# Kernel tuning notes

Measured on AMD Instinct MI355X. Metric: run time of the kernel, lower is better.

## Reference

```python
import jax, jax.numpy as jnp
import numpy as np

HEADS = 8
DIM = 512
DIM_HEAD = DIM // 8        # 64
M = DIM // 2               # 256 landmarks
PINV_ITERS = 6
KERNEL = 33                # residual depthwise conv kernel (33,1)


def moore_penrose_pinv(x, iters):
    # x: [b, h, m, m]; Newton-Schulz style iterative pseudoinverse (lucidrains impl)
    abs_x = jnp.abs(x)
    col = abs_x.sum(axis=-1)
    row = abs_x.sum(axis=-2)
    z = jnp.swapaxes(x, -1, -2) / (jnp.max(col) * jnp.max(row))
    I = jnp.eye(x.shape[-1], dtype=x.dtype)
    for _ in range(iters):
        xz = x @ z
        z = 0.25 * z @ (13.0 * I - xz @ (15.0 * I - xz @ (7.0 * I - xz)))
    return z


def setup_inputs() -> dict:
    key = jax.random.key(0)
    ks = jax.random.split(key, 5)
    b, n, dim = 4, 8192, DIM
    x = jax.random.normal(ks[0], (b, n, dim), dtype=jnp.float32)
    # to_qkv: Linear(dim, 3*inner_dim, bias=False); inner_dim = heads*dim_head = dim
    w_qkv = jax.random.normal(ks[1], (dim, 3 * dim), dtype=jnp.float32) / np.sqrt(dim)
    # to_out: Linear(inner_dim, dim) with bias (dropout = identity in eval)
    w_out = jax.random.normal(ks[2], (dim, dim), dtype=jnp.float32) / np.sqrt(dim)
    b_out = jax.random.normal(ks[3], (dim,), dtype=jnp.float32) * 0.01
    # res_conv: Conv2d(heads, heads, (33,1), padding=(16,0), groups=heads, bias=False)
    conv_w = jax.random.normal(ks[4], (HEADS, 1, KERNEL, 1), dtype=jnp.float32) / np.sqrt(KERNEL)
    return {"x": x, "w_qkv": w_qkv, "w_out": w_out, "b_out": b_out, "conv_w": conv_w}


def nystrom_attention(x, w_qkv, w_out, b_out, conv_w):
    b, n, dim = x.shape
    h, d, m = HEADS, DIM_HEAD, M
    # pad front so seq len divisible by num_landmarks (no-op for n=8192, m=256)
    pad = (m - n % m) % m
    xp = jnp.pad(x, ((0, 0), (pad, 0), (0, 0)))
    np_ = n + pad

    qkv = xp @ w_qkv                                   # [b, np, 3*dim]
    q, k, v = jnp.split(qkv, 3, axis=-1)
    to_heads = lambda t: t.reshape(b, np_, h, d).transpose(0, 2, 1, 3)  # [b,h,np,d]
    q, k, v = to_heads(q), to_heads(k), to_heads(v)
    q = q * (d ** -0.5)

    l = np_ // m                                       # tokens per landmark
    pool = lambda t: t.reshape(b, h, m, l, d).mean(axis=3)  # [b,h,m,d]
    q_l, k_l = pool(q), pool(k)

    attn1 = jax.nn.softmax(jnp.einsum('bhnd,bhmd->bhnm', q, k_l), axis=-1)    # [b,h,np,m]
    attn2 = jax.nn.softmax(jnp.einsum('bhid,bhjd->bhij', q_l, k_l), axis=-1)  # [b,h,m,m]
    attn3 = jax.nn.softmax(jnp.einsum('bhmd,bhnd->bhmn', q_l, k), axis=-1)    # [b,h,m,np]

    attn2_inv = moore_penrose_pinv(attn2, PINV_ITERS)
    out = (attn1 @ attn2_inv) @ (attn3 @ v)            # [b,h,np,d]

    # depthwise conv residual over the sequence axis, per head
    res = jax.lax.conv_general_dilated(
        v, conv_w, window_strides=(1, 1),
        padding=((KERNEL // 2, KERNEL // 2), (0, 0)),
        dimension_numbers=('NCHW', 'OIHW', 'NCHW'),
        feature_group_count=h)
    out = out + res

    out = out.transpose(0, 2, 1, 3).reshape(b, np_, dim)
    out = out @ w_out + b_out
    return out[:, -n:]


def reference(x, w_qkv, w_out, b_out, conv_w):
    return x + nystrom_attention(x, w_qkv, w_out, b_out, conv_w)
```

## Files before the change

### kernel.cpp

```cpp
#include <hip/hip_runtime.h>


#define N_SEQ 8192
#define DMODEL 512
#define NHEAD 8
#define DHEAD 64
#define NLAND 256
#define BH 32

typedef unsigned short u16;
typedef __attribute__((ext_vector_type(8))) short bh8;
typedef __attribute__((ext_vector_type(4))) float fx4;

__device__ __forceinline__ float bf2f(u16 u) { return __uint_as_float(((unsigned)u) << 16); }
__device__ __forceinline__ u16 f2bf(float f) {
    unsigned x = __float_as_uint(f);
    return (u16)((x + 0x7fffu + ((x >> 16) & 1u)) >> 16);
}
__device__ __forceinline__ fx4 mfma16(bh8 a, bh8 b, fx4 c) {
    return __builtin_amdgcn_mfma_f32_16x16x32_bf16(a, b, c, 0, 0, 0);
}
__device__ __forceinline__ void gload16(u16* lds, const u16* g) {
    __builtin_amdgcn_global_load_lds(
        (const __attribute__((address_space(1))) unsigned int*)g,
        (__attribute__((address_space(3))) unsigned int*)lds, 16, 0, 0);
}

__global__ void detect_kernel(const u16* __restrict__ X, unsigned* scal)
{
    __shared__ int cnt;
    if (threadIdx.x == 0) cnt = 0;
    if (threadIdx.x == 0) scal[0] = 0x3f800000u;
    if (threadIdx.x == 1) scal[1] = 0u;
    __syncthreads();
    u16 u = X[threadIdx.x * 2];
    int e = (u >> 7) & 0xFF;
    int insane = (u != 0) && (e < 90 || e > 140);
    atomicAdd(&cnt, insane);
    __syncthreads();
    if (threadIdx.x == 0) scal[2] = (cnt > 64) ? 1u : 0u;
}

__global__ __launch_bounds__(256) void convert4_kernel(
    const void* __restrict__ in, u16* __restrict__ out, int n4, const unsigned* __restrict__ flag)
{
    int i = blockIdx.x * 256 + threadIdx.x;
    if (i >= n4) return;
    if (flag[0]) {
        float4 v = ((const float4*)in)[i];
        ushort4 o;
        o.x = f2bf(v.x); o.y = f2bf(v.y); o.z = f2bf(v.z); o.w = f2bf(v.w);
        ((ushort4*)out)[i] = o;
    } else {
        ((ushort4*)out)[i] = ((const ushort4*)in)[i];
    }
}

__global__ void small_convert_kernel(
    const void* __restrict__ b_in, u16* __restrict__ b_out,
    const void* __restrict__ c_in, u16* __restrict__ c_out,
    const unsigned* __restrict__ flag)
{
    int t = threadIdx.x;
    unsigned f = flag[0];
    const void* in; u16* out; int i;
    if (t < 128)       { in = b_in; out = b_out; i = t; }
    else if (t < 194)  { in = c_in; out = c_out; i = t - 128; }
    else return;
    if (f) {
        float4 v = ((const float4*)in)[i];
        ushort4 o;
        o.x = f2bf(v.x); o.y = f2bf(v.y); o.z = f2bf(v.z); o.w = f2bf(v.w);
        ((ushort4*)out)[i] = o;
    } else {
        ((ushort4*)out)[i] = ((const ushort4*)in)[i];
    }
}

__global__ __launch_bounds__(256) void wtrans2_kernel(
    const void* __restrict__ in1, u16* __restrict__ out1,
    const void* __restrict__ in2, u16* __restrict__ out2,
    const unsigned* __restrict__ flag)
{
    int idx = blockIdx.x * 256 + threadIdx.x;
    unsigned f = flag[0];
    if (idx < 786432) {
        int r = idx / 1536, c = idx % 1536;
        float v = f ? ((const float*)in1)[idx] : bf2f(((const u16*)in1)[idx]);
        out1[(size_t)c * 512 + r] = f2bf(v);
    } else {
        int k = idx - 786432;
        int r = k >> 9, c = k & 511;
        float v = f ? ((const float*)in2)[k] : bf2f(((const u16*)in2)[k]);
        out2[(size_t)c * 512 + r] = f2bf(v);
    }
}

__global__ __launch_bounds__(256) void qkv_mfma_kernel(
    const u16* __restrict__ X, const u16* __restrict__ WT,
    u16* __restrict__ Q, u16* __restrict__ K, u16* __restrict__ VT)
{
    __shared__ __align__(16) u16 SH[128 * 136 + 64];
    u16* Xs = SH;
    u16* Ws = SH + 8192;
    const int tid = threadIdx.x;
    const int wave = tid >> 6, lane = tid & 63;
    const int wrow = (wave >> 1) * 64, wcol = (wave & 1) * 64;
    const int i0 = blockIdx.x * 128;
    const int j0 = blockIdx.y * 128;
    const int la = lane >> 3, lb = lane & 7;
    const int lm = lane & 15, lq = lane >> 4;
    const int sw = lm & 7;
    const int sc = (lb ^ la) * 8;
    fx4 acc[4][4];
#pragma unroll
    for (int a = 0; a < 4; ++a)
#pragma unroll
        for (int b = 0; b < 4; ++b) acc[a][b] = (fx4){0.f, 0.f, 0.f, 0.f};

    for (int k0 = 0; k0 < DMODEL; k0 += 64) {
        __syncthreads();
#pragma unroll
        for (int jj = 0; jj < 4; ++jj) {
            int rb = wave * 32 + jj * 8;
            gload16(Xs + rb * 64, X + (size_t)(i0 + rb + la) * DMODEL + k0 + sc);
            gload16(Ws + rb * 64, WT + (size_t)(j0 + rb + la) * DMODEL + k0 + sc);
        }
        __syncthreads();
#pragma unroll
        for (int ks = 0; ks < 2; ++ks) {
            const int po = ((ks * 4 + lq) ^ sw) * 8;
            bh8 xf[4], wf[4];
#pragma unroll
            for (int im = 0; im < 4; ++im)
                xf[im] = *(const bh8*)(Xs + (wrow + im * 16 + lm) * 64 + po);
#pragma unroll
            for (int in = 0; in < 4; ++in)
                wf[in] = *(const bh8*)(Ws + (wcol + in * 16 + lm) * 64 + po);
#pragma unroll
            for (int im = 0; im < 4; ++im)
#pragma unroll
                for (int in = 0; in < 4; ++in)
                    acc[im][in] = mfma16(wf[in], xf[im], acc[im][in]);
        }
    }

    const int j0V = j0 - 1024;
    if (j0V >= 0) {
        __syncthreads();
#pragma unroll
        for (int im = 0; im < 4; ++im) {
            int nl = wrow + im * 16 + lm;
#pragma unroll
            for (int in = 0; in < 4; ++in) {
                int cl = wcol + in * 16 + (lq << 2);
#pragma unroll
                for (int r = 0; r < 4; ++r)
                    SH[(cl + r) * 136 + nl] = f2bf(acc[im][in][r]);
            }
        }
        __syncthreads();
        const int bb = i0 >> 13, ns0 = i0 & (N_SEQ - 1);
        const size_t rowg0 = (size_t)bb * 512 + j0V;
        const int nof = (tid & 15) * 8;
        const int c0 = tid >> 4;
#pragma unroll
        for (int j = 0; j < 8; ++j) {
            int c = c0 + j * 16;
            uint4 v = *(const uint4*)(SH + c * 136 + nof);
            *(uint4*)(VT + (rowg0 + c) * N_SEQ + ns0 + nof) = v;
        }
    } else {
#pragma unroll
        for (int im = 0; im < 4; ++im) {
            int m = i0 + wrow + im * 16 + lm;
            int bb = m >> 13, ns = m & (N_SEQ - 1);
#pragma unroll
            for (int in = 0; in < 4; ++in) {
                int nn = j0 + wcol + in * 16 + (lq << 2);
                int which = nn >> 9;
                int h = (nn >> 6) & 7;
                int d = nn & 63;
                u16* dst = (which == 0) ? Q : K;
                float s = (which == 0) ? 0.125f : 1.f;
                ushort4 o;
                o.x = f2bf(acc[im][in][0] * s); o.y = f2bf(acc[im][in][1] * s);
                o.z = f2bf(acc[im][in][2] * s); o.w = f2bf(acc[im][in][3] * s);
                *(ushort4*)(dst + ((size_t)(bb * NHEAD + h) * N_SEQ + ns) * DHEAD + d) = o;
            }
        }
    }
}

__global__ __launch_bounds__(64) void pool_kernel(
    const u16* __restrict__ Q, const u16* __restrict__ K,
    float* __restrict__ QL, float* __restrict__ KL,
    u16* __restrict__ QLb, u16* __restrict__ KLb)
{
    int m = blockIdx.x, bh = blockIdx.y, d = threadIdx.x;
    size_t base = ((size_t)bh * N_SEQ + m * 32) * DHEAD + d;
    float sq = 0.f, sk = 0.f;
#pragma unroll
    for (int i = 0; i < 32; ++i) {
        sq += bf2f(Q[base + i * DHEAD]);
        sk += bf2f(K[base + i * DHEAD]);
    }
    size_t ob = ((size_t)bh * NLAND + m) * DHEAD + d;
    sq *= (1.f / 32.f); sk *= (1.f / 32.f);
    QL[ob] = sq; KL[ob] = sk;
    QLb[ob] = f2bf(sq); KLb[ob] = f2bf(sk);
}

__global__ __launch_bounds__(256) void attn2_kernel(
    const float* __restrict__ QL, const float* __restrict__ KL, float* __restrict__ A2)
{
    __shared__ float qrow[64];
    __shared__ float red[256];
    int i = blockIdx.x, bh = blockIdx.y, j = threadIdx.x;
    if (j < 64) qrow[j] = QL[((size_t)bh * NLAND + i) * DHEAD + j];
    __syncthreads();
    const float* kr = KL + ((size_t)bh * NLAND + j) * DHEAD;
    float lg = 0.f;
#pragma unroll
    for (int d = 0; d < 64; ++d) lg += qrow[d] * kr[d];
    red[j] = lg; __syncthreads();
    for (int s = 128; s > 0; s >>= 1) { if (j < s) red[j] = fmaxf(red[j], red[j + s]); __syncthreads(); }
    float mx = red[0]; __syncthreads();
    float p = __expf(lg - mx);
    red[j] = p; __syncthreads();
    for (int s = 128; s > 0; s >>= 1) { if (j < s) red[j] += red[j + s]; __syncthreads(); }
    float sum = red[0];
    A2[((size_t)bh * NLAND + i) * NLAND + j] = p / sum;
}

__global__ __launch_bounds__(256) void absmax_kernel(const float* __restrict__ A2, unsigned* scal)
{
    __shared__ float red[256];
    int bh = blockIdx.x, t = threadIdx.x;
    const float* Ab = A2 + (size_t)bh * 65536;
    float rs = 0.f;
    for (int i = 0; i < 256; ++i) rs += fabsf(Ab[i * 256 + t]);
    red[t] = rs; __syncthreads();
    for (int s = 128; s > 0; s >>= 1) { if (t < s) red[t] = fmaxf(red[t], red[t + s]); __syncthreads(); }
    if (t == 0) atomicMax(scal + 1, __float_as_uint(red[0]));
}

__global__ __launch_bounds__(256) void z0_kernel(
    const float* __restrict__ A2, const unsigned* __restrict__ scal,
    u16* __restrict__ zb, u16* __restrict__ zbT, u16* __restrict__ A2b)
{
    float inv = 1.f / (__uint_as_float(scal[0]) * __uint_as_float(scal[1]));
    size_t idx = (size_t)blockIdx.x * 256 + threadIdx.x;
    size_t bh = idx >> 16;
    int r = (int)(idx & 65535);
    int i = r >> 8, j = r & 255;
    float a = A2[idx];
    zb[idx]  = f2bf(A2[(bh << 16) + (size_t)j * 256 + i] * inv);
    zbT[idx] = f2bf(a * inv);
    A2b[idx] = f2bf(a);
}

__global__ __launch_bounds__(256) void bgemm_mfma_kernel(
    const u16* __restrict__ A, const u16* __restrict__ BT,
    u16* __restrict__ Cn, u16* __restrict__ Ct, const u16* __restrict__ E,
    int N, long sB, long sCn, long sCt, float sc, float alpha, float beta, int wn, int wt)
{
    __shared__ u16 As[64 * 72];
    __shared__ u16 Bs[64 * 72];
    const int tid = threadIdx.x;
    const int wave = tid >> 6, lane = tid & 63;
    const int wm = (wave >> 1) * 32, wnn = (wave & 1) * 32;
    const int i0 = blockIdx.x * 64, j0 = blockIdx.y * 64, bh = blockIdx.z;
    const u16* Ab = A + (size_t)bh * 65536;
    const u16* Bb = BT + (size_t)bh * sB;
    const int srow = tid >> 2, scol = (tid & 3) * 16;
    const int lm = lane & 15, lq = lane >> 4;
    fx4 acc[2][2];
#pragma unroll
    for (int a = 0; a < 2; ++a)
#pragma unroll
        for (int b = 0; b < 2; ++b) acc[a][b] = (fx4){0.f, 0.f, 0.f, 0.f};

    for (int k0 = 0; k0 < 256; k0 += 64) {
        uint4 a0 = *(const uint4*)(Ab + (size_t)(i0 + srow) * 256 + k0 + scol);
        uint4 a1 = *(const uint4*)(Ab + (size_t)(i0 + srow) * 256 + k0 + scol + 8);
        uint4 b0 = *(const uint4*)(Bb + (size_t)(j0 + srow) * 256 + k0 + scol);
        uint4 b1 = *(const uint4*)(Bb + (size_t)(j0 + srow) * 256 + k0 + scol + 8);
        __syncthreads();
        *(uint4*)(As + srow * 72 + scol) = a0;
        *(uint4*)(As + srow * 72 + scol + 8) = a1;
        *(uint4*)(Bs + srow * 72 + scol) = b0;
        *(uint4*)(Bs + srow * 72 + scol + 8) = b1;
        __syncthreads();
#pragma unroll
        for (int ks = 0; ks < 2; ++ks) {
            bh8 lf[2], rf[2];
#pragma unroll
            for (int im = 0; im < 2; ++im)
                lf[im] = *(const bh8*)(As + (wm + im * 16 + lm) * 72 + ks * 32 + lq * 8);
#pragma unroll
            for (int in = 0; in < 2; ++in)
                rf[in] = *(const bh8*)(Bs + (wnn + in * 16 + lm) * 72 + ks * 32 + lq * 8);
#pragma unroll
            for (int im = 0; im < 2; ++im)
#pragma unroll
                for (int in = 0; in < 2; ++in)
                    acc[im][in] = mfma16(lf[im], rf[in], acc[im][in]);
        }
    }
#pragma unroll
    for (int im = 0; im < 2; ++im) {
#pragma unroll
        for (int in = 0; in < 2; ++in) {
            int n = j0 + wnn + in * 16 + lm;
            int m0 = i0 + wm + im * 16 + (lq << 2);
            float c[4];
#pragma unroll
            for (int r = 0; r < 4; ++r) {
                int m = m0 + r;
                float x = beta * acc[im][in][r];
                if (alpha != 0.f)
                    x += alpha * bf2f(E[(size_t)bh * 65536 + (size_t)m * 256 + n]);
                if (m == n) x += sc;
                c[r] = x;
            }
            if (wn) {
#pragma unroll
                for (int r = 0; r < 4; ++r)
                    Cn[(size_t)bh * sCn + (size_t)(m0 + r) * N + n] = f2bf(c[r]);
            }
            if (wt) {
                ushort4 o;
                o.x = f2bf(c[0]); o.y = f2bf(c[1]); o.z = f2bf(c[2]); o.w = f2bf(c[3]);
                *(ushort4*)(Ct + (size_t)bh * sCt + (size_t)n * 256 + m0) = o;
            }
        }
    }
}

__global__ __launch_bounds__(256) void bgemm_pair_kernel(
    const u16* __restrict__ Az, const u16* __restrict__ Au, const u16* __restrict__ BT,
    u16* __restrict__ Czn, u16* __restrict__ Cun, u16* __restrict__ CunT)
{
    __shared__ u16 As[64 * 72];
    __shared__ u16 Bs[64 * 72];
    const int tid = threadIdx.x;
    const int wave = tid >> 6, lane = tid & 63;
    const int wm = (wave >> 1) * 32, wnn = (wave & 1) * 32;
    const int i0 = blockIdx.x * 64, j0 = blockIdx.y * 64;
    const int bz = blockIdx.z;
    const int bh = bz & 31;
    const int isU = bz >> 5;
    const u16* Ab = (isU ? Au : Az) + (size_t)bh * 65536;
    const u16* Bb = BT + (size_t)bh * 65536;
    const int srow = tid >> 2, scol = (tid & 3) * 16;
    const int lm = lane & 15, lq = lane >> 4;
    fx4 acc[2][2];
#pragma unroll
    for (int a = 0; a < 2; ++a)
#pragma unroll
        for (int b = 0; b < 2; ++b) acc[a][b] = (fx4){0.f, 0.f, 0.f, 0.f};

    for (int k0 = 0; k0 < 256; k0 += 64) {
        uint4 a0 = *(const uint4*)(Ab + (size_t)(i0 + srow) * 256 + k0 + scol);
        uint4 a1 = *(const uint4*)(Ab + (size_t)(i0 + srow) * 256 + k0 + scol + 8);
        uint4 b0 = *(const uint4*)(Bb + (size_t)(j0 + srow) * 256 + k0 + scol);
        uint4 b1 = *(const uint4*)(Bb + (size_t)(j0 + srow) * 256 + k0 + scol + 8);
        __syncthreads();
        *(uint4*)(As + srow * 72 + scol) = a0;
        *(uint4*)(As + srow * 72 + scol + 8) = a1;
        *(uint4*)(Bs + srow * 72 + scol) = b0;
        *(uint4*)(Bs + srow * 72 + scol + 8) = b1;
        __syncthreads();
#pragma unroll
        for (int ks = 0; ks < 2; ++ks) {
            bh8 lf[2], rf[2];
#pragma unroll
            for (int im = 0; im < 2; ++im)
                lf[im] = *(const bh8*)(As + (wm + im * 16 + lm) * 72 + ks * 32 + lq * 8);
#pragma unroll
            for (int in = 0; in < 2; ++in)
                rf[in] = *(const bh8*)(Bs + (wnn + in * 16 + lm) * 72 + ks * 32 + lq * 8);
#pragma unroll
            for (int im = 0; im < 2; ++im)
#pragma unroll
                for (int in = 0; in < 2; ++in)
                    acc[im][in] = mfma16(lf[im], rf[in], acc[im][in]);
        }
    }
#pragma unroll
    for (int im = 0; im < 2; ++im) {
#pragma unroll
        for (int in = 0; in < 2; ++in) {
            int n = j0 + wnn + in * 16 + lm;
            int m0 = i0 + wm + im * 16 + (lq << 2);
            float c[4];
#pragma unroll
            for (int r = 0; r < 4; ++r) c[r] = 0.25f * acc[im][in][r];
            u16* rows = isU ? Cun : Czn;
#pragma unroll
            for (int r = 0; r < 4; ++r)
                rows[(size_t)bh * 65536 + (size_t)(m0 + r) * 256 + n] = f2bf(c[r]);
            if (isU) {
                ushort4 o;
                o.x = f2bf(c[0]); o.y = f2bf(c[1]); o.z = f2bf(c[2]); o.w = f2bf(c[3]);
                *(ushort4*)(CunT + (size_t)bh * 65536 + (size_t)n * 256 + m0) = o;
            }
        }
    }
}

__global__ __launch_bounds__(256, 2) void attn3v_mfma_kernel(
    const u16* __restrict__ QLb, const u16* __restrict__ Kb,
    const u16* __restrict__ VTb, u16* __restrict__ PO, float* __restrict__ ML)
{
    __shared__ u16 Ks[64 * 72];
    __shared__ u16 Vs[64 * 72];
    __shared__ u16 Pw[4][64 * 72];
    const int tid = threadIdx.x;
    const int wave = tid >> 6, lane = tid & 63;
    const int q = lane >> 4, l15 = lane & 15;
    const int part = blockIdx.x;
    const int bh = blockIdx.y;
    const int nbase = part * 512;
    const int srow = tid >> 2, scol = (tid & 3) * 16;
    u16* Pp = Pw[wave];
    bh8 qf[4][2];
#pragma unroll
    for (int mt = 0; mt < 4; ++mt)
#pragma unroll
        for (int ks = 0; ks < 2; ++ks)
            qf[mt][ks] = *(const bh8*)(QLb + ((size_t)bh * NLAND + wave * 64 + mt * 16 + l15) * DHEAD + ks * 32 + q * 8);
    float M[4] = {-1e30f, -1e30f, -1e30f, -1e30f};
    float L[4] = {0.f, 0.f, 0.f, 0.f};
    fx4 O[4][4];
#pragma unroll
    for (int mt = 0; mt < 4; ++mt)
#pragma unroll
        for (int dt = 0; dt < 4; ++dt) O[mt][dt] = (fx4){0.f, 0.f, 0.f, 0.f};

    for (int c = 0; c < 8; ++c) {
        const int n0 = nbase + c * 64;
        uint4 k0v = *(const uint4*)(Kb + ((size_t)bh * N_SEQ + n0 + srow) * DHEAD + scol);
        uint4 k1v = *(const uint4*)(Kb + ((size_t)bh * N_SEQ + n0 + srow) * DHEAD + scol + 8);
        uint4 v0v = *(const uint4*)(VTb + ((size_t)bh * DHEAD + srow) * N_SEQ + n0 + scol);
        uint4 v1v = *(const uint4*)(VTb + ((size_t)bh * DHEAD + srow) * N_SEQ + n0 + scol + 8);
        __syncthreads();
        *(uint4*)(Ks + srow * 72 + scol) = k0v;
        *(uint4*)(Ks + srow * 72 + scol + 8) = k1v;
        *(uint4*)(Vs + srow * 72 + scol) = v0v;
        *(uint4*)(Vs + srow * 72 + scol + 8) = v1v;
        __syncthreads();
        fx4 S[4][4];
#pragma unroll
        for (int nt = 0; nt < 4; ++nt)
#pragma unroll
            for (int mt = 0; mt < 4; ++mt) S[nt][mt] = (fx4){0.f, 0.f, 0.f, 0.f};
#pragma unroll
        for (int ks = 0; ks < 2; ++ks) {
            bh8 kf[4];
#pragma unroll
            for (int nt = 0; nt < 4; ++nt)
                kf[nt] = *(const bh8*)(Ks + (nt * 16 + l15) * 72 + ks * 32 + q * 8);
#pragma unroll
            for (int nt = 0; nt < 4; ++nt)
#pragma unroll
                for (int mt = 0; mt < 4; ++mt)
                    S[nt][mt] = mfma16(kf[nt], qf[mt][ks], S[nt][mt]);
        }
#pragma unroll
        for (int mt = 0; mt < 4; ++mt) {
            float cm = -1e30f;
#pragma unroll
            for (int nt = 0; nt < 4; ++nt)
#pragma unroll
                for (int r = 0; r < 4; ++r) cm = fmaxf(cm, S[nt][mt][r]);
            cm = fmaxf(cm, __shfl_xor(cm, 16));
            cm = fmaxf(cm, __shfl_xor(cm, 32));
            float Mn = fmaxf(M[mt], cm);
            float al = __expf(M[mt] - Mn);
            M[mt] = Mn;
            L[mt] *= al;
#pragma unroll
            for (int dt = 0; dt < 4; ++dt) {
                O[mt][dt][0] *= al; O[mt][dt][1] *= al;
                O[mt][dt][2] *= al; O[mt][dt][3] *= al;
            }
            float ps = 0.f;
#pragma unroll
            for (int nt = 0; nt < 4; ++nt)
#pragma unroll
                for (int r = 0; r < 4; ++r) {
                    float p = __expf(S[nt][mt][r] - Mn);
                    ps += p;
                    Pp[(mt * 16 + l15) * 72 + nt * 16 + q * 4 + r] = f2bf(p);
                }
            ps += __shfl_xor(ps, 16);
            ps += __shfl_xor(ps, 32);
            L[mt] += ps;
        }
#pragma unroll
        for (int ks = 0; ks < 2; ++ks) {
            bh8 pf[4];
#pragma unroll
            for (int mt = 0; mt < 4; ++mt)
                pf[mt] = *(const bh8*)(Pp + (mt * 16 + l15) * 72 + ks * 32 + q * 8);
#pragma unroll
            for (int dt = 0; dt < 4; ++dt) {
                bh8 vf = *(const bh8*)(Vs + (dt * 16 + l15) * 72 + ks * 32 + q * 8);
#pragma unroll
                for (int mt = 0; mt < 4; ++mt)
                    O[mt][dt] = mfma16(vf, pf[mt], O[mt][dt]);
            }
        }
    }
#pragma unroll
    for (int mt = 0; mt < 4; ++mt) {
        size_t mrow = (size_t)(bh * 16 + part) * NLAND + wave * 64 + mt * 16 + l15;
#pragma unroll
        for (int dt = 0; dt < 4; ++dt) {
            ushort4 o;
            o.x = f2bf(O[mt][dt][0]); o.y = f2bf(O[mt][dt][1]);
            o.z = f2bf(O[mt][dt][2]); o.w = f2bf(O[mt][dt][3]);
            *(ushort4*)(PO + mrow * DHEAD + dt * 16 + q * 4) = o;
        }
        if (q == 0) { ML[mrow * 2] = M[mt]; ML[mrow * 2 + 1] = L[mt]; }
    }
}

__global__ __launch_bounds__(64) void combine_kernel(
    const u16* __restrict__ PO, const float* __restrict__ ML, u16* __restrict__ W3VT)
{
    int m = blockIdx.x, bh = blockIdx.y, d = threadIdx.x;
    float Mg = -1e30f;
#pragma unroll
    for (int p = 0; p < 16; ++p)
        Mg = fmaxf(Mg, ML[((size_t)(bh * 16 + p) * NLAND + m) * 2]);
    float denom = 0.f, o = 0.f;
#pragma unroll
    for (int p = 0; p < 16; ++p) {
        size_t ix = (size_t)(bh * 16 + p) * NLAND + m;
        float w = __expf(ML[ix * 2] - Mg);
        denom += ML[ix * 2 + 1] * w;
        o += bf2f(PO[ix * DHEAD + d]) * w;
    }
    W3VT[((size_t)bh * DHEAD + d) * NLAND + m] = f2bf(o / denom);
}

__global__ __launch_bounds__(256) void conv_kernel(
    const u16* __restrict__ VT, const u16* __restrict__ CW, u16* __restrict__ RT)
{
    __shared__ float vl[2080];
    __shared__ float cws[33];
    const int tid = threadIdx.x;
    const int c0 = blockIdx.x * 2048;
    const int row = blockIdx.y;
    const int h = (row >> 6) & 7;
    const u16* src = VT + (size_t)row * N_SEQ;
    for (int i = tid; i < 2080; i += 256) {
        int gn = c0 - 16 + i;
        vl[i] = (gn >= 0 && gn < N_SEQ) ? bf2f(src[gn]) : 0.f;
    }
    if (tid < 33) cws[tid] = bf2f(CW[h * 33 + tid]);
    __syncthreads();
    float v[40];
    const int base = tid * 8;
#pragma unroll
    for (int i = 0; i < 40; ++i) v[i] = vl[base + i];
    float s[8];
#pragma unroll
    for (int j = 0; j < 8; ++j) {
        float a = 0.f;
#pragma unroll
        for (int t = 0; t < 33; ++t) a += cws[t] * v[j + t];
        s[j] = a;
    }
    u16* dst = RT + (size_t)row * N_SEQ + c0 + base;
    ushort4 o0, o1;
    o0.x = f2bf(s[0]); o0.y = f2bf(s[1]); o0.z = f2bf(s[2]); o0.w = f2bf(s[3]);
    o1.x = f2bf(s[4]); o1.y = f2bf(s[5]); o1.z = f2bf(s[6]); o1.w = f2bf(s[7]);
    *(ushort4*)dst = o0;
    *(ushort4*)(dst + 4) = o1;
}

__global__ __launch_bounds__(256) void outheads_mfma_kernel(
    const u16* __restrict__ Qb, const u16* __restrict__ KLb,
    const u16* __restrict__ WMT, const u16* __restrict__ RT,
    u16* __restrict__ Y)
{
    __shared__ u16 Pl[64 * 264];
    __shared__ float wmax[4][64];
    __shared__ float wsum[4][64];
    const int tid = threadIdx.x;
    const int wave = tid >> 6, lane = tid & 63;
    const int q = lane >> 4, l15 = lane & 15;
    const int bh = blockIdx.y;
    const int bb = bh >> 3, h = bh & 7;
    const int n0 = blockIdx.x * 64;
    fx4 S[4][4];
#pragma unroll
    for (int a = 0; a < 4; ++a)
#pragma unroll
        for (int b = 0; b < 4; ++b) S[a][b] = (fx4){0.f, 0.f, 0.f, 0.f};
#pragma unroll
    for (int ks = 0; ks < 2; ++ks) {
        bh8 qfr[4];
#pragma unroll
        for (int nt = 0; nt < 4; ++nt)
            qfr[nt] = *(const bh8*)(Qb + ((size_t)bh * N_SEQ + n0 + nt * 16 + l15) * DHEAD + ks * 32 + q * 8);
#pragma unroll
        for (int mt = 0; mt < 4; ++mt) {
            bh8 kf = *(const bh8*)(KLb + ((size_t)bh * NLAND + wave * 64 + mt * 16 + l15) * DHEAD + ks * 32 + q * 8);
#pragma unroll
            for (int nt = 0; nt < 4; ++nt)
                S[nt][mt] = mfma16(qfr[nt], kf, S[nt][mt]);
        }
    }
#pragma unroll
    for (int nt = 0; nt < 4; ++nt)
#pragma unroll
        for (int r = 0; r < 4; ++r) {
            float pm = fmaxf(fmaxf(S[nt][0][r], S[nt][1][r]), fmaxf(S[nt][2][r], S[nt][3][r]));
            pm = fmaxf(pm, __shfl_xor(pm, 1));
            pm = fmaxf(pm, __shfl_xor(pm, 2));
            pm = fmaxf(pm, __shfl_xor(pm, 4));
            pm = fmaxf(pm, __shfl_xor(pm, 8));
            if (l15 == 0) wmax[wave][nt * 16 + q * 4 + r] = pm;
        }
    __syncthreads();
#pragma unroll
    for (int nt = 0; nt < 4; ++nt)
#pragma unroll
        for (int r = 0; r < 4; ++r) {
            int nl = nt * 16 + q * 4 + r;
            float Mf = fmaxf(fmaxf(wmax[0][nl], wmax[1][nl]), fmaxf(wmax[2][nl], wmax[3][nl]));
            float ps = 0.f;
#pragma unroll
            for (int mt = 0; mt < 4; ++mt) {
                float p = __expf(S[nt][mt][r] - Mf);
                ps += p;
                Pl[nl * 264 + wave * 64 + mt * 16 + l15] = f2bf(p);
            }
            ps += __shfl_xor(ps, 1);
            ps += __shfl_xor(ps, 2);
            ps += __shfl_xor(ps, 4);
            ps += __shfl_xor(ps, 8);
            if (l15 == 0) wsum[wave][nl] = ps;
        }
    __syncthreads();
    fx4 O[4];
#pragma unroll
    for (int nt = 0; nt < 4; ++nt) O[nt] = (fx4){0.f, 0.f, 0.f, 0.f};
#pragma unroll
    for (int ks = 0; ks < 8; ++ks) {
        bh8 af = *(const bh8*)(WMT + ((size_t)bh * DHEAD + wave * 16 + l15) * NLAND + ks * 32 + q * 8);
#pragma unroll
        for (int nt = 0; nt < 4; ++nt) {
            bh8 pf = *(const bh8*)(Pl + (size_t)(nt * 16 + l15) * 264 + ks * 32 + q * 8);
            O[nt] = mfma16(af, pf, O[nt]);
        }
    }
#pragma unroll
    for (int nt = 0; nt < 4; ++nt) {
        int nl = nt * 16 + l15;
        float inv = 1.f / (wsum[0][nl] + wsum[1][nl] + wsum[2][nl] + wsum[3][nl]);
        int d0 = wave * 16 + (q << 2);
        fx4 v = O[nt];
#pragma unroll
        for (int c = 0; c < 4; ++c)
            v[c] = v[c] * inv + bf2f(RT[(size_t)(bh * DHEAD + d0 + c) * N_SEQ + n0 + nl]);
        ushort4 o;
        o.x = f2bf(v[0]); o.y = f2bf(v[1]); o.z = f2bf(v[2]); o.w = f2bf(v[3]);
        *(ushort4*)(Y + ((size_t)bb * N_SEQ + n0 + nl) * DMODEL + h * DHEAD + d0) = o;
    }
}

__global__ __launch_bounds__(256) void final_mfma_kernel(
    const u16* __restrict__ Y, const u16* __restrict__ WT,
    const u16* __restrict__ Bias, const u16* __restrict__ X, void* __restrict__ Out,
    const unsigned* __restrict__ flag)
{
    __shared__ u16 Xs[128 * 64];
    __shared__ u16 Ws[128 * 64];
    const int tid = threadIdx.x;
    const int wave = tid >> 6, lane = tid & 63;
    const int wrow = (wave >> 1) * 64, wcol = (wave & 1) * 64;
    const int i0 = blockIdx.x * 128;
    const int j0 = blockIdx.y * 128;
    const int la = lane >> 3, lb = lane & 7;
    const int lm = lane & 15, lq = lane >> 4;
    const int sw = lm & 7;
    const int sc = (lb ^ la) * 8;
    const unsigned isf32 = flag[0];
    fx4 acc[4][4];
#pragma unroll
    for (int a = 0; a < 4; ++a)
#pragma unroll
        for (int b = 0; b < 4; ++b) acc[a][b] = (fx4){0.f, 0.f, 0.f, 0.f};

    for (int k0 = 0; k0 < DMODEL; k0 += 64) {
        __syncthreads();
#pragma unroll
        for (int jj = 0; jj < 4; ++jj) {
            int rb = wave * 32 + jj * 8;
            gload16(Xs + rb * 64, Y + (size_t)(i0 + rb + la) * DMODEL + k0 + sc);
            gload16(Ws + rb * 64, WT + (size_t)(j0 + rb + la) * DMODEL + k0 + sc);
        }
        __syncthreads();
#pragma unroll
        for (int ks = 0; ks < 2; ++ks) {
            const int po = ((ks * 4 + lq) ^ sw) * 8;
            bh8 xf[4], wf[4];
#pragma unroll
            for (int im = 0; im < 4; ++im)
                xf[im] = *(const bh8*)(Xs + (wrow + im * 16 + lm) * 64 + po);
#pragma unroll
            for (int in = 0; in < 4; ++in)
                wf[in] = *(const bh8*)(Ws + (wcol + in * 16 + lm) * 64 + po);
#pragma unroll
            for (int im = 0; im < 4; ++im)
#pragma unroll
                for (int in = 0; in < 4; ++in)
                    acc[im][in] = mfma16(wf[in], xf[im], acc[im][in]);
        }
    }
#pragma unroll
    for (int im = 0; im < 4; ++im) {
        int m = i0 + wrow + im * 16 + lm;
#pragma unroll
        for (int in = 0; in < 4; ++in) {
            int nn = j0 + wcol + in * 16 + (lq << 2);
            ushort4 b4 = *(const ushort4*)(Bias + nn);
            ushort4 x4 = *(const ushort4*)(X + (size_t)m * DMODEL + nn);
            float c0 = acc[im][in][0] + bf2f(b4.x) + bf2f(x4.x);
            float c1 = acc[im][in][1] + bf2f(b4.y) + bf2f(x4.y);
            float c2 = acc[im][in][2] + bf2f(b4.z) + bf2f(x4.z);
            float c3 = acc[im][in][3] + bf2f(b4.w) + bf2f(x4.w);
            if (isf32) {
                *(float4*)((float*)Out + (size_t)m * DMODEL + nn) = make_float4(c0, c1, c2, c3);
            } else {
                ushort4 o;
                o.x = f2bf(c0); o.y = f2bf(c1); o.z = f2bf(c2); o.w = f2bf(c3);
                *(ushort4*)((u16*)Out + (size_t)m * DMODEL + nn) = o;
            }
        }
    }
}

extern "C" void kernel_launch(void* const* d_in, const int* in_sizes, int n_in,
                              void* d_out, int out_size, void* d_ws, size_t ws_size,
                              hipStream_t stream)
{
    (void)in_sizes; (void)n_in; (void)out_size; (void)ws_size;
    char* ws = (char*)d_ws;
    u16*   Xc    = (u16*)(ws + 0);
    u16*   WqkvT = (u16*)(ws + 33554432);
    u16*   WoutT = (u16*)(ws + 35127296);
    u16*   Boutc = (u16*)(ws + 35651584);
    u16*   CWc   = (u16*)(ws + 35652608);
    u16*   Qb    = (u16*)(ws + 35653632);
    u16*   Kb    = (u16*)(ws + 69208064);
    u16*   RT    = (u16*)(ws + 69208064);
    u16*   VTb   = (u16*)(ws + 102762496);
    float* QL    = (float*)(ws + 136316928);
    float* KL    = (float*)(ws + 138414080);
    u16*   QLb   = (u16*)(ws + 140511232);
    u16*   KLb   = (u16*)(ws + 141559808);
    u16*   W3VT  = (u16*)(ws + 142608384);
    u16*   WMT   = (u16*)(ws + 143656960);
    u16*   A2b   = (u16*)(ws + 144705536);
    u16*   zA    = (u16*)(ws + 148899840);
    u16*   zAT   = (u16*)(ws + 153094144);
    float* A2    = (float*)(ws + 157288448);
    u16*   PO    = (u16*)(ws + 157288448);
    float* ML    = (float*)(ws + 174065664);
    u16*   zB    = (u16*)(ws + 165677056);
    u16*   zBT   = (u16*)(ws + 169871360);
    u16*   xz    = (u16*)(ws + 174065664);
    u16*   xzT   = (u16*)(ws + 178259968);
    u16*   t2T   = (u16*)(ws + 182454272);
    u16*   t3T   = (u16*)(ws + 186648576);
    u16*   Yb    = (u16*)(ws + 157288448);
    unsigned* SCAL = (unsigned*)(ws + 190842880);

    detect_kernel<<<1, 256, 0, stream>>>((const u16*)d_in[0], SCAL);
    convert4_kernel<<<16384, 256, 0, stream>>>(d_in[0], Xc, 4194304, SCAL + 2);
    wtrans2_kernel<<<4096, 256, 0, stream>>>(d_in[1], WqkvT, d_in[2], WoutT, SCAL + 2);
    small_convert_kernel<<<1, 256, 0, stream>>>(d_in[3], Boutc, d_in[4], CWc, SCAL + 2);

    qkv_mfma_kernel<<<dim3(256, 12), 256, 0, stream>>>(Xc, WqkvT, Qb, Kb, VTb);
    pool_kernel<<<dim3(256, BH), 64, 0, stream>>>(Qb, Kb, QL, KL, QLb, KLb);
    attn2_kernel<<<dim3(256, BH), 256, 0, stream>>>(QL, KL, A2);
    absmax_kernel<<<32, 256, 0, stream>>>(A2, SCAL);
    z0_kernel<<<8192, 256, 0, stream>>>(A2, SCAL, zA, zAT, A2b);

    attn3v_mfma_kernel<<<dim3(16, BH), 256, 0, stream>>>(QLb, Kb, VTb, PO, ML);
    combine_kernel<<<dim3(256, BH), 64, 0, stream>>>(PO, ML, W3VT);
    conv_kernel<<<dim3(4, 2048), 256, 0, stream>>>(VTb, CWc, RT);

    u16 *z = zA, *zn = zB;
    u16 *u = xz, *uT = xzT, *un = zAT, *unT = zBT;
    bgemm_mfma_kernel<<<dim3(4, 4, 32), 256, 0, stream>>>(
        A2b, zAT, u, uT, A2b, 256, 65536, 65536, 65536, 0.f, 0.f, 1.f, 1, 1);
    for (int it = 0; it < 6; ++it) {
        bgemm_mfma_kernel<<<dim3(4, 4, 32), 256, 0, stream>>>(
            u, uT, u, t2T, u, 256, 65536, 65536, 65536, 15.f, -7.f, 1.f, 0, 1);
        bgemm_mfma_kernel<<<dim3(4, 4, 32), 256, 0, stream>>>(
            u, t2T, u, t3T, u, 256, 65536, 65536, 65536, 13.f, 0.f, -1.f, 0, 1);
        bgemm_pair_kernel<<<dim3(4, 4, 64), 256, 0, stream>>>(
            z, u, t3T, zn, un, unT);
        u16* tp;
        tp = z;  z = zn;  zn = tp;
        tp = u;  u = un;  un = tp;
        tp = uT; uT = unT; unT = tp;
    }
    bgemm_mfma_kernel<<<dim3(4, 1, 32), 256, 0, stream>>>(
        z, W3VT, WMT, WMT, A2b, 64, 16384, 16384, 16384, 0.f, 0.f, 1.f, 0, 1);

    outheads_mfma_kernel<<<dim3(128, BH), 256, 0, stream>>>(Qb, KLb, WMT, RT, Yb);
    final_mfma_kernel<<<dim3(256, 4), 256, 0, stream>>>(Yb, WoutT, Boutc, Xc, d_out, SCAL + 2);
}
```

Measured before the change: 697.9 us.

## Fuse pinv polynomial GEMMs, merge conv into attn3v, and merge preprocessing kernels

Replaces the two chained GEMMs per Newton-Schulz iteration with one kernel that computes U², applies a factored cubic polynomial in LDS, and multiplies by U again, removing the t2T intermediate round trip and a launch. The depthwise conv is merged into the attn3v kernel through block-index dispatch, and the three input conversion kernels become one launch. The fused pinv kernel launches far fewer blocks (128), which lowers parallelism, and its factored constants change the rounding behaviour.

```diff
diff --git a/kernel.cpp b/kernel.cpp
--- a/kernel.cpp
+++ b/kernel.cpp
@@ -41,58 +41,51 @@
     if (threadIdx.x == 0) scal[2] = (cnt > 64) ? 1u : 0u;
 }
 
-__global__ __launch_bounds__(256) void convert4_kernel(
-    const void* __restrict__ in, u16* __restrict__ out, int n4, const unsigned* __restrict__ flag)
-{
-    int i = blockIdx.x * 256 + threadIdx.x;
-    if (i >= n4) return;
-    if (flag[0]) {
-        float4 v = ((const float4*)in)[i];
-        ushort4 o;
-        o.x = f2bf(v.x); o.y = f2bf(v.y); o.z = f2bf(v.z); o.w = f2bf(v.w);
-        ((ushort4*)out)[i] = o;
+__global__ __launch_bounds__(256) void preproc_kernel(
+    const void* __restrict__ x_in, u16* __restrict__ Xc,
+    const void* __restrict__ w1_in, u16* __restrict__ W1T,
+    const void* __restrict__ w2_in, u16* __restrict__ W2T,
+    const void* __restrict__ b_in, u16* __restrict__ Bout,
+    const void* __restrict__ c_in, u16* __restrict__ Cout,
+    const unsigned* __restrict__ flag)
+{
+    const int bid = blockIdx.x, tid = threadIdx.x;
+    const unsigned f = flag[0];
+    if (bid < 16384) {
+        int i = bid * 256 + tid;
+        if (f) {
+            float4 v = ((const float4*)x_in)[i];
+            ushort4 o;
+            o.x = f2bf(v.x); o.y = f2bf(v.y); o.z = f2bf(v.z); o.w = f2bf(v.w);
+            ((ushort4*)Xc)[i] = o;
+        } else {
+            ((ushort4*)Xc)[i] = ((const ushort4*)x_in)[i];
+        }
+    } else if (bid < 20480) {
+        int idx = (bid - 16384) * 256 + tid;
+        if (idx < 786432) {
+            int r = idx / 1536, c = idx % 1536;
+            float v = f ? ((const float*)w1_in)[idx] : bf2f(((const u16*)w1_in)[idx]);
+            W1T[(size_t)c * 512 + r] = f2bf(v);
+        } else {
+            int k = idx - 786432;
+            int r = k >> 9, c = k & 511;
+            float v = f ? ((const float*)w2_in)[k] : bf2f(((const u16*)w2_in)[k]);
+            W2T[(size_t)c * 512 + r] = f2bf(v);
+        }
     } else {
-        ((ushort4*)out)[i] = ((const ushort4*)in)[i];
-    }
-}
-
-__global__ void small_convert_kernel(
-    const void* __restrict__ b_in, u16* __restrict__ b_out,
-    const void* __restrict__ c_in, u16* __restrict__ c_out,
-    const unsigned* __restrict__ flag)
-{
-    int t = threadIdx.x;
-    unsigned f = flag[0];
-    const void* in; u16* out; int i;
-    if (t < 128)       { in = b_in; out = b_out; i = t; }
-    else if (t < 194)  { in = c_in; out = c_out; i = t - 128; }
-    else return;
-    if (f) {
-        float4 v = ((const float4*)in)[i];
-        ushort4 o;
-        o.x = f2bf(v.x); o.y = f2bf(v.y); o.z = f2bf(v.z); o.w = f2bf(v.w);
-        ((ushort4*)out)[i] = o;
-    } else {
-        ((ushort4*)out)[i] = ((const ushort4*)in)[i];
-    }
-}
-
-__global__ __launch_bounds__(256) void wtrans2_kernel(
-    const void* __restrict__ in1, u16* __restrict__ out1,
-    const void* __restrict__ in2, u16* __restrict__ out2,
-    const unsigned* __restrict__ flag)
-{
-    int idx = blockIdx.x * 256 + threadIdx.x;
-    unsigned f = flag[0];
-    if (idx < 786432) {
-        int r = idx / 1536, c = idx % 1536;
-        float v = f ? ((const float*)in1)[idx] : bf2f(((const u16*)in1)[idx]);
-        out1[(size_t)c * 512 + r] = f2bf(v);
-    } else {
-        int k = idx - 786432;
-        int r = k >> 9, c = k & 511;
-        float v = f ? ((const float*)in2)[k] : bf2f(((const u16*)in2)[k]);
-        out2[(size_t)c * 512 + r] = f2bf(v);
+        const void* in; u16* out; int i;
+        if (tid < 128)       { in = b_in; out = Bout; i = tid; }
+        else if (tid < 194)  { in = c_in; out = Cout; i = tid - 128; }
+        else return;
+        if (f) {
+            float4 v = ((const float4*)in)[i];
+            ushort4 o;
+            o.x = f2bf(v.x); o.y = f2bf(v.y); o.z = f2bf(v.z); o.w = f2bf(v.w);
+            ((ushort4*)out)[i] = o;
+        } else {
+            ((ushort4*)out)[i] = ((const ushort4*)in)[i];
+        }
     }
 }
 
@@ -335,6 +328,122 @@
                 *(ushort4*)(Ct + (size_t)bh * sCt + (size_t)n * 256 + m0) = o;
             }
         }
+    }
+}
+
+__global__ __launch_bounds__(256) void t2t3_fused_kernel(
+    const u16* __restrict__ U, const u16* __restrict__ UT, u16* __restrict__ T3T)
+{
+    __shared__ u16 Qs[64 * 264];
+    __shared__ u16 As[64 * 72];
+    __shared__ u16 Bs[64 * 72];
+    const float FB = 4.1304f, FG = -2.8696f, FD = 3.1474f;
+    const int tid = threadIdx.x;
+    const int wave = tid >> 6, lane = tid & 63;
+    const int wm = (wave >> 1) * 32, wnn = (wave & 1) * 32;
+    const int i0 = blockIdx.x * 64, bh = blockIdx.y;
+    const u16* Ub = U + (size_t)bh * 65536;
+    const u16* UTb = UT + (size_t)bh * 65536;
+    const int srow = tid >> 2, scol = (tid & 3) * 16;
+    const int lm = lane & 15, lq = lane >> 4;
+
+#pragma unroll 1
+    for (int jt = 0; jt < 4; ++jt) {
+        const int j0 = jt * 64;
+        fx4 acc[2][2];
+#pragma unroll
+        for (int a = 0; a < 2; ++a)
+#pragma unroll
+            for (int b = 0; b < 2; ++b) acc[a][b] = (fx4){0.f, 0.f, 0.f, 0.f};
+        for (int k0 = 0; k0 < 256; k0 += 64) {
+            uint4 a0 = *(const uint4*)(Ub + (size_t)(i0 + srow) * 256 + k0 + scol);
+            uint4 a1 = *(const uint4*)(Ub + (size_t)(i0 + srow) * 256 + k0 + scol + 8);
+            uint4 b0 = *(const uint4*)(UTb + (size_t)(j0 + srow) * 256 + k0 + scol);
+            uint4 b1 = *(const uint4*)(UTb + (size_t)(j0 + srow) * 256 + k0 + scol + 8);
+            __syncthreads();
+            *(uint4*)(As + srow * 72 + scol) = a0;
+            *(uint4*)(As + srow * 72 + scol + 8) = a1;
+            *(uint4*)(Bs + srow * 72 + scol) = b0;
+            *(uint4*)(Bs + srow * 72 + scol + 8) = b1;
+            __syncthreads();
+#pragma unroll
+            for (int ks = 0; ks < 2; ++ks) {
+                bh8 lf[2], rf[2];
+#pragma unroll
+                for (int im = 0; im < 2; ++im)
+                    lf[im] = *(const bh8*)(As + (wm + im * 16 + lm) * 72 + ks * 32 + lq * 8);
+#pragma unroll
+                for (int in = 0; in < 2; ++in)
+                    rf[in] = *(const bh8*)(Bs + (wnn + in * 16 + lm) * 72 + ks * 32 + lq * 8);
+#pragma unroll
+                for (int im = 0; im < 2; ++im)
+#pragma unroll
+                    for (int in = 0; in < 2; ++in)
+                        acc[im][in] = mfma16(lf[im], rf[in], acc[im][in]);
+            }
+        }
+#pragma unroll
+        for (int im = 0; im < 2; ++im)
+#pragma unroll
+            for (int in = 0; in < 2; ++in) {
+                int n = j0 + wnn + in * 16 + lm;
+                int m0 = i0 + wm + im * 16 + (lq << 2);
+#pragma unroll
+                for (int r = 0; r < 4; ++r) {
+                    int m = m0 + r;
+                    float x = acc[im][in][r] + FG * bf2f(Ub[(size_t)m * 256 + n]);
+                    if (m == n) x += FD;
+                    Qs[(m - i0) * 264 + n] = f2bf(x);
+                }
+            }
+    }
+    __syncthreads();
+
+#pragma unroll 1
+    for (int jt = 0; jt < 4; ++jt) {
+        const int j0 = jt * 64;
+        fx4 acc[2][2];
+#pragma unroll
+        for (int a = 0; a < 2; ++a)
+#pragma unroll
+            for (int b = 0; b < 2; ++b) acc[a][b] = (fx4){0.f, 0.f, 0.f, 0.f};
+        for (int k0 = 0; k0 < 256; k0 += 64) {
+            uint4 b0 = *(const uint4*)(UTb + (size_t)(j0 + srow) * 256 + k0 + scol);
+            uint4 b1 = *(const uint4*)(UTb + (size_t)(j0 + srow) * 256 + k0 + scol + 8);
+            __syncthreads();
+            *(uint4*)(Bs + srow * 72 + scol) = b0;
+            *(uint4*)(Bs + srow * 72 + scol + 8) = b1;
+            __syncthreads();
+#pragma unroll
+            for (int ks = 0; ks < 2; ++ks) {
+                bh8 lf[2], rf[2];
+#pragma unroll
+                for (int im = 0; im < 2; ++im)
+                    lf[im] = *(const bh8*)(Qs + (wm + im * 16 + lm) * 264 + k0 + ks * 32 + lq * 8);
+#pragma unroll
+                for (int in = 0; in < 2; ++in)
+                    rf[in] = *(const bh8*)(Bs + (wnn + in * 16 + lm) * 72 + ks * 32 + lq * 8);
+#pragma unroll
+                for (int im = 0; im < 2; ++im)
+#pragma unroll
+                    for (int in = 0; in < 2; ++in)
+                        acc[im][in] = mfma16(lf[im], rf[in], acc[im][in]);
+            }
+        }
+#pragma unroll
+        for (int im = 0; im < 2; ++im)
+#pragma unroll
+            for (int in = 0; in < 2; ++in) {
+                int n = j0 + wnn + in * 16 + lm;
+                int m0 = i0 + wm + im * 16 + (lq << 2);
+                ushort4 o;
+#pragma unroll
+                for (int r = 0; r < 4; ++r) {
+                    float ql = bf2f(Qs[(m0 - i0 + r) * 264 + n]);
+                    ((u16*)&o)[r] = f2bf(FB * ql - acc[im][in][r]);
+                }
+                *(ushort4*)(T3T + (size_t)bh * 65536 + (size_t)n * 256 + m0) = o;
+            }
     }
 }
 
@@ -410,121 +519,165 @@
     }
 }
 
-__global__ __launch_bounds__(256, 2) void attn3v_mfma_kernel(
+__global__ __launch_bounds__(256) void attn3v_conv_kernel(
     const u16* __restrict__ QLb, const u16* __restrict__ Kb,
-    const u16* __restrict__ VTb, u16* __restrict__ PO, float* __restrict__ ML)
-{
-    __shared__ u16 Ks[64 * 72];
-    __shared__ u16 Vs[64 * 72];
-    __shared__ u16 Pw[4][64 * 72];
+    const u16* __restrict__ VTb, u16* __restrict__ PO, float* __restrict__ ML,
+    const u16* __restrict__ CW, u16* __restrict__ RT)
+{
+    __shared__ __align__(16) char POOL[55296];
+    const int bid = blockIdx.x;
     const int tid = threadIdx.x;
-    const int wave = tid >> 6, lane = tid & 63;
-    const int q = lane >> 4, l15 = lane & 15;
-    const int part = blockIdx.x;
-    const int bh = blockIdx.y;
-    const int nbase = part * 512;
-    const int srow = tid >> 2, scol = (tid & 3) * 16;
-    u16* Pp = Pw[wave];
-    bh8 qf[4][2];
-#pragma unroll
-    for (int mt = 0; mt < 4; ++mt)
-#pragma unroll
-        for (int ks = 0; ks < 2; ++ks)
-            qf[mt][ks] = *(const bh8*)(QLb + ((size_t)bh * NLAND + wave * 64 + mt * 16 + l15) * DHEAD + ks * 32 + q * 8);
-    float M[4] = {-1e30f, -1e30f, -1e30f, -1e30f};
-    float L[4] = {0.f, 0.f, 0.f, 0.f};
-    fx4 O[4][4];
-#pragma unroll
-    for (int mt = 0; mt < 4; ++mt)
-#pragma unroll
-        for (int dt = 0; dt < 4; ++dt) O[mt][dt] = (fx4){0.f, 0.f, 0.f, 0.f};
-
-    for (int c = 0; c < 8; ++c) {
-        const int n0 = nbase + c * 64;
-        uint4 k0v = *(const uint4*)(Kb + ((size_t)bh * N_SEQ + n0 + srow) * DHEAD + scol);
-        uint4 k1v = *(const uint4*)(Kb + ((size_t)bh * N_SEQ + n0 + srow) * DHEAD + scol + 8);
-        uint4 v0v = *(const uint4*)(VTb + ((size_t)bh * DHEAD + srow) * N_SEQ + n0 + scol);
-        uint4 v1v = *(const uint4*)(VTb + ((size_t)bh * DHEAD + srow) * N_SEQ + n0 + scol + 8);
-        __syncthreads();
-        *(uint4*)(Ks + srow * 72 + scol) = k0v;
-        *(uint4*)(Ks + srow * 72 + scol + 8) = k1v;
-        *(uint4*)(Vs + srow * 72 + scol) = v0v;
-        *(uint4*)(Vs + srow * 72 + scol + 8) = v1v;
-        __syncthreads();
-        fx4 S[4][4];
-#pragma unroll
-        for (int nt = 0; nt < 4; ++nt)
-#pragma unroll
-            for (int mt = 0; mt < 4; ++mt) S[nt][mt] = (fx4){0.f, 0.f, 0.f, 0.f};
-#pragma unroll
-        for (int ks = 0; ks < 2; ++ks) {
-            bh8 kf[4];
+    int aidx = -1, cidx;
+    if (bid < 8192) {
+        if ((bid & 15) == 0) aidx = bid >> 4;
+        else cidx = bid - (bid >> 4) - 1;
+    } else {
+        cidx = bid - 512;
+    }
+
+    if (aidx >= 0) {
+        u16* Ks = (u16*)POOL;
+        u16* Vs = Ks + 4608;
+        u16* PwB = Vs + 4608;
+        const int wave = tid >> 6, lane = tid & 63;
+        const int q = lane >> 4, l15 = lane & 15;
+        const int part = aidx & 15;
+        const int bh = aidx >> 4;
+        const int nbase = part * 512;
+        const int srow = tid >> 2, scol = (tid & 3) * 16;
+        u16* Pp = PwB + wave * 4608;
+        bh8 qf[4][2];
+#pragma unroll
+        for (int mt = 0; mt < 4; ++mt)
+#pragma unroll
+            for (int ks = 0; ks < 2; ++ks)
+                qf[mt][ks] = *(const bh8*)(QLb + ((size_t)bh * NLAND + wave * 64 + mt * 16 + l15) * DHEAD + ks * 32 + q * 8);
+        float M[4] = {-1e30f, -1e30f, -1e30f, -1e30f};
+        float L[4] = {0.f, 0.f, 0.f, 0.f};
+        fx4 O[4][4];
+#pragma unroll
+        for (int mt = 0; mt < 4; ++mt)
+#pragma unroll
+            for (int dt = 0; dt < 4; ++dt) O[mt][dt] = (fx4){0.f, 0.f, 0.f, 0.f};
+
+        for (int c = 0; c < 8; ++c) {
+            const int n0 = nbase + c * 64;
+            uint4 k0v = *(const uint4*)(Kb + ((size_t)bh * N_SEQ + n0 + srow) * DHEAD + scol);
+            uint4 k1v = *(const uint4*)(Kb + ((size_t)bh * N_SEQ + n0 + srow) * DHEAD + scol + 8);
+            uint4 v0v = *(const uint4*)(VTb + ((size_t)bh * DHEAD + srow) * N_SEQ + n0 + scol);
+            uint4 v1v = *(const uint4*)(VTb + ((size_t)bh * DHEAD + srow) * N_SEQ + n0 + scol + 8);
+            __syncthreads();
+            *(uint4*)(Ks + srow * 72 + scol) = k0v;
+            *(uint4*)(Ks + srow * 72 + scol + 8) = k1v;
+            *(uint4*)(Vs + srow * 72 + scol) = v0v;
+            *(uint4*)(Vs + srow * 72 + scol + 8) = v1v;
+            __syncthreads();
+            fx4 S[4][4];
 #pragma unroll
             for (int nt = 0; nt < 4; ++nt)
-                kf[nt] = *(const bh8*)(Ks + (nt * 16 + l15) * 72 + ks * 32 + q * 8);
-#pragma unroll
-            for (int nt = 0; nt < 4; ++nt)
+#pragma unroll
+                for (int mt = 0; mt < 4; ++mt) S[nt][mt] = (fx4){0.f, 0.f, 0.f, 0.f};
+#pragma unroll
+            for (int ks = 0; ks < 2; ++ks) {
+                bh8 kf[4];
+#pragma unroll
+                for (int nt = 0; nt < 4; ++nt)
+                    kf[nt] = *(const bh8*)(Ks + (nt * 16 + l15) * 72 + ks * 32 + q * 8);
+#pragma unroll
+                for (int nt = 0; nt < 4; ++nt)
+#pragma unroll
+                    for (int mt = 0; mt < 4; ++mt)
+                        S[nt][mt] = mfma16(kf[nt], qf[mt][ks], S[nt][mt]);
+            }
+#pragma unroll
+            for (int mt = 0; mt < 4; ++mt) {
+                float cm = -1e30f;
+#pragma unroll
+                for (int nt = 0; nt < 4; ++nt)
+#pragma unroll
+                    for (int r = 0; r < 4; ++r) cm = fmaxf(cm, S[nt][mt][r]);
+                cm = fmaxf(cm, __shfl_xor(cm, 16));
+                cm = fmaxf(cm, __shfl_xor(cm, 32));
+                float Mn = fmaxf(M[mt], cm);
+                float al = __expf(M[mt] - Mn);
+                M[mt] = Mn;
+                L[mt] *= al;
+#pragma unroll
+                for (int dt = 0; dt < 4; ++dt) {
+                    O[mt][dt][0] *= al; O[mt][dt][1] *= al;
+                    O[mt][dt][2] *= al; O[mt][dt][3] *= al;
+                }
+                float ps = 0.f;
+#pragma unroll
+                for (int nt = 0; nt < 4; ++nt)
+#pragma unroll
+                    for (int r = 0; r < 4; ++r) {
+                        float p = __expf(S[nt][mt][r] - Mn);
+                        ps += p;
+                        Pp[(mt * 16 + l15) * 72 + nt * 16 + q * 4 + r] = f2bf(p);
+                    }
+                ps += __shfl_xor(ps, 16);
+                ps += __shfl_xor(ps, 32);
+                L[mt] += ps;
+            }
+#pragma unroll
+            for (int ks = 0; ks < 2; ++ks) {
+                bh8 pf[4];
 #pragma unroll
                 for (int mt = 0; mt < 4; ++mt)
-                    S[nt][mt] = mfma16(kf[nt], qf[mt][ks], S[nt][mt]);
+                    pf[mt] = *(const bh8*)(Pp + (mt * 16 + l15) * 72 + ks * 32 + q * 8);
+#pragma unroll
+                for (int dt = 0; dt < 4; ++dt) {
+                    bh8 vf = *(const bh8*)(Vs + (dt * 16 + l15) * 72 + ks * 32 + q * 8);
+#pragma unroll
+                    for (int mt = 0; mt < 4; ++mt)
+                        O[mt][dt] = mfma16(vf, pf[mt], O[mt][dt]);
+                }
+            }
         }
 #pragma unroll
         for (int mt = 0; mt < 4; ++mt) {
-            float cm = -1e30f;
-#pragma unroll
-            for (int nt = 0; nt < 4; ++nt)
-#pragma unroll
-                for (int r = 0; r < 4; ++r) cm = fmaxf(cm, S[nt][mt][r]);
-            cm = fmaxf(cm, __shfl_xor(cm, 16));
-            cm = fmaxf(cm, __shfl_xor(cm, 32));
-            float Mn = fmaxf(M[mt], cm);
-            float al = __expf(M[mt] - Mn);
-            M[mt] = Mn;
-            L[mt] *= al;
+            size_t mrow = (size_t)(bh * 16 + part) * NLAND + wave * 64 + mt * 16 + l15;
 #pragma unroll
             for (int dt = 0; dt < 4; ++dt) {
-                O[mt][dt][0] *= al; O[mt][dt][1] *= al;
-                O[mt][dt][2] *= al; O[mt][dt][3] *= al;
-            }
-            float ps = 0.f;
-#pragma unroll
-            for (int nt = 0; nt < 4; ++nt)
-#pragma unroll
-                for (int r = 0; r < 4; ++r) {
-                    float p = __expf(S[nt][mt][r] - Mn);
-                    ps += p;
-                    Pp[(mt * 16 + l15) * 72 + nt * 16 + q * 4 + r] = f2bf(p);
-                }
-            ps += __shfl_xor(ps, 16);
-            ps += __shfl_xor(ps, 32);
-            L[mt] += ps;
-        }
-#pragma unroll
-        for (int ks = 0; ks < 2; ++ks) {
-            bh8 pf[4];
-#pragma unroll
-            for (int mt = 0; mt < 4; ++mt)
-                pf[mt] = *(const bh8*)(Pp + (mt * 16 + l15) * 72 + ks * 32 + q * 8);
-#pragma unroll
-            for (int dt = 0; dt < 4; ++dt) {
-                bh8 vf = *(const bh8*)(Vs + (dt * 16 + l15) * 72 + ks * 32 + q * 8);
-#pragma unroll
-                for (int mt = 0; mt < 4; ++mt)
-                    O[mt][dt] = mfma16(vf, pf[mt], O[mt][dt]);
-            }
-        }
-    }
-#pragma unroll
-    for (int mt = 0; mt < 4; ++mt) {
-        size_t mrow = (size_t)(bh * 16 + part) * NLAND + wave * 64 + mt * 16 + l15;
-#pragma unroll
-        for (int dt = 0; dt < 4; ++dt) {
-            ushort4 o;
-            o.x = f2bf(O[mt][dt][0]); o.y = f2bf(O[mt][dt][1]);
-            o.z = f2bf(O[mt][dt][2]); o.w = f2bf(O[mt][dt][3]);
-            *(ushort4*)(PO + mrow * DHEAD + dt * 16 + q * 4) = o;
-        }
-        if (q == 0) { ML[mrow * 2] = M[mt]; ML[mrow * 2 + 1] = L[mt]; }
+                ushort4 o;
+                o.x = f2bf(O[mt][dt][0]); o.y = f2bf(O[mt][dt][1]);
+                o.z = f2bf(O[mt][dt][2]); o.w = f2bf(O[mt][dt][3]);
+                *(ushort4*)(PO + mrow * DHEAD + dt * 16 + q * 4) = o;
+            }
+            if (q == 0) { ML[mrow * 2] = M[mt]; ML[mrow * 2 + 1] = L[mt]; }
+        }
+    } else {
+        float* vl = (float*)POOL;
+        float* cws = vl + 2080;
+        const int c0 = (cidx & 3) * 2048;
+        const int row = cidx >> 2;
+        const int h = (row >> 6) & 7;
+        const u16* src = VTb + (size_t)row * N_SEQ;
+        for (int i = tid; i < 2080; i += 256) {
+            int gn = c0 - 16 + i;
+            vl[i] = (gn >= 0 && gn < N_SEQ) ? bf2f(src[gn]) : 0.f;
+        }
+        if (tid < 33) cws[tid] = bf2f(CW[h * 33 + tid]);
+        __syncthreads();
+        float v[40];
+        const int base = tid * 8;
+#pragma unroll
+        for (int i = 0; i < 40; ++i) v[i] = vl[base + i];
+        float s[8];
+#pragma unroll
+        for (int j = 0; j < 8; ++j) {
+            float a = 0.f;
+#pragma unroll
+            for (int t = 0; t < 33; ++t) a += cws[t] * v[j + t];
+            s[j] = a;
+        }
+        u16* dst = RT + (size_t)row * N_SEQ + c0 + base;
+        ushort4 o0, o1;
+        o0.x = f2bf(s[0]); o0.y = f2bf(s[1]); o0.z = f2bf(s[2]); o0.w = f2bf(s[3]);
+        o1.x = f2bf(s[4]); o1.y = f2bf(s[5]); o1.z = f2bf(s[6]); o1.w = f2bf(s[7]);
+        *(ushort4*)dst = o0;
+        *(ushort4*)(dst + 4) = o1;
     }
 }
 
@@ -545,42 +698,6 @@
         o += bf2f(PO[ix * DHEAD + d]) * w;
     }
     W3VT[((size_t)bh * DHEAD + d) * NLAND + m] = f2bf(o / denom);
-}
-
-__global__ __launch_bounds__(256) void conv_kernel(
-    const u16* __restrict__ VT, const u16* __restrict__ CW, u16* __restrict__ RT)
-{
-    __shared__ float vl[2080];
-    __shared__ float cws[33];
-    const int tid = threadIdx.x;
-    const int c0 = blockIdx.x * 2048;
-    const int row = blockIdx.y;
-    const int h = (row >> 6) & 7;
-    const u16* src = VT + (size_t)row * N_SEQ;
-    for (int i = tid; i < 2080; i += 256) {
-        int gn = c0 - 16 + i;
-        vl[i] = (gn >= 0 && gn < N_SEQ) ? bf2f(src[gn]) : 0.f;
-    }
-    if (tid < 33) cws[tid] = bf2f(CW[h * 33 + tid]);
-    __syncthreads();
-    float v[40];
-    const int base = tid * 8;
-#pragma unroll
-    for (int i = 0; i < 40; ++i) v[i] = vl[base + i];
-    float s[8];
-#pragma unroll
-    for (int j = 0; j < 8; ++j) {
-        float a = 0.f;
-#pragma unroll
-        for (int t = 0; t < 33; ++t) a += cws[t] * v[j + t];
-        s[j] = a;
-    }
-    u16* dst = RT + (size_t)row * N_SEQ + c0 + base;
-    ushort4 o0, o1;
-    o0.x = f2bf(s[0]); o0.y = f2bf(s[1]); o0.z = f2bf(s[2]); o0.w = f2bf(s[3]);
-    o1.x = f2bf(s[4]); o1.y = f2bf(s[5]); o1.z = f2bf(s[6]); o1.w = f2bf(s[7]);
-    *(ushort4*)dst = o0;
-    *(ushort4*)(dst + 4) = o1;
 }
 
 __global__ __launch_bounds__(256) void outheads_mfma_kernel(
@@ -778,15 +895,13 @@
     u16*   zBT   = (u16*)(ws + 169871360);
     u16*   xz    = (u16*)(ws + 174065664);
     u16*   xzT   = (u16*)(ws + 178259968);
-    u16*   t2T   = (u16*)(ws + 182454272);
     u16*   t3T   = (u16*)(ws + 186648576);
     u16*   Yb    = (u16*)(ws + 157288448);
     unsigned* SCAL = (unsigned*)(ws + 190842880);
 
     detect_kernel<<<1, 256, 0, stream>>>((const u16*)d_in[0], SCAL);
-    convert4_kernel<<<16384, 256, 0, stream>>>(d_in[0], Xc, 4194304, SCAL + 2);
-    wtrans2_kernel<<<4096, 256, 0, stream>>>(d_in[1], WqkvT, d_in[2], WoutT, SCAL + 2);
-    small_convert_kernel<<<1, 256, 0, stream>>>(d_in[3], Boutc, d_in[4], CWc, SCAL + 2);
+    preproc_kernel<<<20481, 256, 0, stream>>>(
+        d_in[0], Xc, d_in[1], WqkvT, d_in[2], WoutT, d_in[3], Boutc, d_in[4], CWc, SCAL + 2);
 
     qkv_mfma_kernel<<<dim3(256, 12), 256, 0, stream>>>(Xc, WqkvT, Qb, Kb, VTb);
     pool_kernel<<<dim3(256, BH), 64, 0, stream>>>(Qb, Kb, QL, KL, QLb, KLb);
@@ -794,19 +909,15 @@
     absmax_kernel<<<32, 256, 0, stream>>>(A2, SCAL);
     z0_kernel<<<8192, 256, 0, stream>>>(A2, SCAL, zA, zAT, A2b);
 
-    attn3v_mfma_kernel<<<dim3(16, BH), 256, 0, stream>>>(QLb, Kb, VTb, PO, ML);
+    attn3v_conv_kernel<<<8704, 256, 0, stream>>>(QLb, Kb, VTb, PO, ML, CWc, RT);
     combine_kernel<<<dim3(256, BH), 64, 0, stream>>>(PO, ML, W3VT);
-    conv_kernel<<<dim3(4, 2048), 256, 0, stream>>>(VTb, CWc, RT);
 
     u16 *z = zA, *zn = zB;
     u16 *u = xz, *uT = xzT, *un = zAT, *unT = zBT;
     bgemm_mfma_kernel<<<dim3(4, 4, 32), 256, 0, stream>>>(
         A2b, zAT, u, uT, A2b, 256, 65536, 65536, 65536, 0.f, 0.f, 1.f, 1, 1);
     for (int it = 0; it < 6; ++it) {
-        bgemm_mfma_kernel<<<dim3(4, 4, 32), 256, 0, stream>>>(
-            u, uT, u, t2T, u, 256, 65536, 65536, 65536, 15.f, -7.f, 1.f, 0, 1);
-        bgemm_mfma_kernel<<<dim3(4, 4, 32), 256, 0, stream>>>(
-            u, t2T, u, t3T, u, 256, 65536, 65536, 65536, 13.f, 0.f, -1.f, 0, 1);
+        t2t3_fused_kernel<<<dim3(4, 32), 256, 0, stream>>>(u, uT, t3T);
         bgemm_pair_kernel<<<dim3(4, 4, 64), 256, 0, stream>>>(
             z, u, t3T, zn, un, unT);
         u16* tp;
```

Result: slower. 1.399 ms (+100.5%).
